# Performance work log

Hardware: AMD Instinct MI355X
Metric: run time of the kernel (lower is better)

## Reference

```python
import jax, jax.numpy as jnp
import numpy as np

N_NODES = 50000
DEG = 32
WIDTH = 128
DEPTH = 2
BATCH = 4096
EPS = 1e-12  # F.normalize default eps


def setup_inputs() -> dict:
    key = jax.random.key(0)
    k1, k2, k3, k4, k5, k6, k7 = jax.random.split(key, 7)
    nbd = jax.random.randint(k1, (N_NODES, DEG), 0, N_NODES, dtype=jnp.int32)
    node_idx = jax.random.randint(k2, (BATCH,), 0, N_NODES, dtype=jnp.int32)
    feats = jax.random.normal(k3, (BATCH, WIDTH), dtype=jnp.float32)
    s = 1.0 / np.sqrt(WIDTH)
    W_agg = jax.random.normal(k4, (WIDTH, WIDTH), dtype=jnp.float32) * s
    b_agg = jax.random.normal(k5, (WIDTH,), dtype=jnp.float32) * s
    W_lin = jax.random.normal(k6, (WIDTH, 2 * WIDTH), dtype=jnp.float32) * s
    b_lin = jax.random.normal(k7, (WIDTH,), dtype=jnp.float32) * s
    return {"nbd": nbd, "node_idx": node_idx, "feats": feats,
            "W_agg": W_agg, "b_agg": b_agg, "W_lin": W_lin, "b_lin": b_lin}


def reference(nbd, node_idx, feats, W_agg, b_agg, W_lin, b_lin):
    # H0: zero features for every graph node except the batch nodes (dict-of-zeros + row assignment in original)
    H = jnp.zeros((N_NODES, WIDTH), dtype=feats.dtype).at[node_idx].set(feats)
    for _ in range(DEPTH):  # combine Linear is weight-shared across hops (ModuleList([layer]*depth))
        # aggregator MLP applied once per node, then gathered per neighbor
        M = jax.nn.relu(H @ W_agg.T + b_agg)            # [N, d]
        agg = jnp.max(M[nbd], axis=1)                    # [N, deg, d] -> [N, d] max-pool aggregate
        h = jax.nn.relu(jnp.concatenate([H, agg], axis=-1) @ W_lin.T + b_lin)  # [N, d]
        norm = jnp.sqrt(jnp.sum(h * h, axis=-1, keepdims=True))
        H = h / jnp.maximum(norm, EPS)                   # F.normalize(dim=0) on 1d vector == per-row l2 norm
    return H[node_idx]                                   # [batch, width]
```

## Files before the change

kernel.cpp:

```cpp
#include <hip/hip_runtime.h>
#include <math.h>

#define N_NODES 50000
#define DEG 32
#define WIDTH 128
#define BATCH 4096
#define EPS 1e-12f

typedef __attribute__((ext_vector_type(8))) short short8;
typedef __attribute__((ext_vector_type(4))) float f32x4;
typedef unsigned short u16;

__device__ __forceinline__ u16 f2bf(float f) {
    unsigned x;
    __builtin_memcpy(&x, &f, 4);
    unsigned r = (x + 0x7fff + ((x >> 16) & 1)) >> 16;
    return (u16)r;
}
__device__ __forceinline__ unsigned pkmax_u16(unsigned a, unsigned b) {
    unsigned lo = (a & 0xffffu) > (b & 0xffffu) ? (a & 0xffffu) : (b & 0xffffu);
    unsigned hi = (a >> 16) > (b >> 16) ? (a >> 16) : (b >> 16);
    return lo | (hi << 16);
}

__global__ void prep_k(const float* __restrict__ W_agg, const float* __restrict__ W_lin,
                       const float* __restrict__ b_agg, int* __restrict__ inv,
                       u16* __restrict__ Wab, u16* __restrict__ Wlb,
                       unsigned* __restrict__ rbap) {
    int i = blockIdx.x * 256 + threadIdx.x;
    if (i < 50048) inv[i] = -1;
    int j = i - 50048;
    if (j >= 0 && j < 16384) Wab[j] = f2bf(W_agg[j]);
    int k = i - (50048 + 16384);
    if (k >= 0 && k < 32768) Wlb[k] = f2bf(W_lin[k]);
    if (i < 64) {
        float a = b_agg[2 * i], b = b_agg[2 * i + 1];
        a = a > 0.f ? a : 0.f;
        b = b > 0.f ? b : 0.f;
        rbap[i] = (unsigned)f2bf(a) | ((unsigned)f2bf(b) << 16);
    }
}

__global__ __launch_bounds__(512) void head_k(
    const float* __restrict__ feats, const u16* __restrict__ Wab, const u16* __restrict__ Wlb,
    const float* __restrict__ b_agg, const int* __restrict__ node_idx, int* __restrict__ inv,
    u16* __restrict__ M0b, float* __restrict__ S) {
    int tid = threadIdx.x;
    int gid = blockIdx.x * 512 + tid;
    if (gid < BATCH) atomicMax(&inv[node_idx[gid]], gid);

    int w = tid >> 6, l = tid & 63, li = l & 15, kq = l >> 4;
    int r0 = blockIdx.x * 16;
    int arow = r0 + li;
    int col = w * 16 + li;

    f32x4 am = (f32x4){0,0,0,0}, as = (f32x4){0,0,0,0};
#pragma unroll
    for (int kk = 0; kk < 4; ++kk) {
        float4 a0 = *(const float4*)(feats + (size_t)arow * 128 + kk * 32 + kq * 8);
        float4 a1 = *(const float4*)(feats + (size_t)arow * 128 + kk * 32 + kq * 8 + 4);
        short8 a;
        a[0] = (short)f2bf(a0.x); a[1] = (short)f2bf(a0.y);
        a[2] = (short)f2bf(a0.z); a[3] = (short)f2bf(a0.w);
        a[4] = (short)f2bf(a1.x); a[5] = (short)f2bf(a1.y);
        a[6] = (short)f2bf(a1.z); a[7] = (short)f2bf(a1.w);
        short8 bm = *(const short8*)(Wab + (size_t)col * 128 + kk * 32 + kq * 8);
        am = __builtin_amdgcn_mfma_f32_16x16x32_bf16(a, bm, am, 0, 0, 0);
        short8 bs = *(const short8*)(Wlb + (size_t)col * 256 + kk * 32 + kq * 8);
        as = __builtin_amdgcn_mfma_f32_16x16x32_bf16(a, bs, as, 0, 0, 0);
    }

    float ba = b_agg[col];
#pragma unroll
    for (int r = 0; r < 4; ++r) {
        int grow = r0 + kq * 4 + r;
        float t = am[r] + ba;
        t = t > 0.f ? t : 0.f;
        M0b[(size_t)grow * 128 + col] = f2bf(t);
        S[(size_t)grow * 128 + col] = as[r];
    }
}

__global__ __launch_bounds__(256) void agg1_k(
    const int* __restrict__ nbd, const int* __restrict__ inv,
    const u16* __restrict__ M0b, const unsigned* __restrict__ rbap,
    unsigned* __restrict__ AGG1u) {
    int wave = blockIdx.x * 4 + (threadIdx.x >> 6);
    int lane = threadIdx.x & 63;
    int n0 = wave * 2;

    int nb = nbd[(size_t)n0 * DEG + lane];
    int bi = inv[nb];
    unsigned long long warm = __ballot(bi >= 0);
    unsigned m0 = (unsigned)warm;
    unsigned m1 = (unsigned)(warm >> 32);

    unsigned rb = rbap[lane];

    unsigned acc0 = (m0 != 0xffffffffu) ? rb : 0u;
    while (m0) {
        int pos = __builtin_ctz(m0);
        m0 &= m0 - 1;
        int bib = __shfl(bi, pos);
        unsigned v = ((const unsigned*)(M0b + (size_t)bib * WIDTH))[lane];
        acc0 = pkmax_u16(acc0, v);
    }
    AGG1u[(size_t)n0 * 64 + lane] = acc0;

    unsigned acc1 = (m1 != 0xffffffffu) ? rb : 0u;
    while (m1) {
        int pos = __builtin_ctz(m1);
        m1 &= m1 - 1;
        int bib = __shfl(bi, 32 + pos);
        unsigned v = ((const unsigned*)(M0b + (size_t)bib * WIDTH))[lane];
        acc1 = pkmax_u16(acc1, v);
    }
    AGG1u[(size_t)(n0 + 1) * 64 + lane] = acc1;
}

__global__ __launch_bounds__(512) void hop1mm_k(
    const u16* __restrict__ AGG1, const int* __restrict__ inv,
    const float* __restrict__ S, const float* __restrict__ b_lin,
    const float* __restrict__ b_agg,
    const u16* __restrict__ Wlb, const u16* __restrict__ Wab,
    u16* __restrict__ H1g, u16* __restrict__ M1) {
    __shared__ u16 wlds[128 * 128];
    __shared__ u16 h1t[128 * 136];

    int tid = threadIdx.x;
    int w = tid >> 6, l = tid & 63, li = l & 15, kq = l >> 4;
    int row0 = blockIdx.x * 128;
    int lrow = w * 16 + li;
    int arow = row0 + lrow;
    if (arow > N_NODES - 1) arow = N_NODES - 1;

    short8 af[4];
#pragma unroll
    for (int kk = 0; kk < 4; ++kk)
        af[kk] = *(const short8*)(AGG1 + (size_t)arow * 128 + kk * 32 + kq * 8);

#pragma unroll
    for (int it = 0; it < 4; ++it) {
        int c = tid + it * 512;
        int r = c >> 4;
        int cb = (c & 15) << 4;
        short8 v = *(const short8*)(Wlb + (size_t)r * 256 + 128 + ((c & 15) << 3));
        *(short8*)((char*)wlds + r * 256 + (cb ^ ((r & 7) << 4))) = v;
    }
    __syncthreads();

    f32x4 h[8];
#pragma unroll
    for (int n = 0; n < 8; ++n) h[n] = (f32x4){0,0,0,0};
#pragma unroll
    for (int kk = 0; kk < 4; ++kk)
#pragma unroll
        for (int n = 0; n < 8; ++n) {
            int col = n * 16 + li;
            short8 b = *(const short8*)((char*)wlds + col * 256 +
                                        ((kk * 64 + kq * 16) ^ ((col & 7) << 4)));
            h[n] = __builtin_amdgcn_mfma_f32_16x16x32_bf16(af[kk], b, h[n], 0, 0, 0);
        }

    float blv[8];
#pragma unroll
    for (int n = 0; n < 8; ++n) blv[n] = b_lin[n * 16 + li];

#pragma unroll
    for (int r = 0; r < 4; ++r) {
        int lr = w * 16 + kq * 4 + r;
        int grow = row0 + lr;
        int growc = grow < N_NODES ? grow : N_NODES - 1;
        int bi = inv[growc];
        float v[8];
#pragma unroll
        for (int n = 0; n < 8; ++n) v[n] = h[n][r] + blv[n];
        if (bi >= 0) {
#pragma unroll
            for (int n = 0; n < 8; ++n) v[n] += S[(size_t)bi * 128 + n * 16 + li];
        }
        float p = 0.f;
#pragma unroll
        for (int n = 0; n < 8; ++n) {
            v[n] = fmaxf(v[n], 0.f);
            p += v[n] * v[n];
        }
        p += __shfl_xor(p, 1);
        p += __shfl_xor(p, 2);
        p += __shfl_xor(p, 4);
        p += __shfl_xor(p, 8);
        float sc = 1.0f / fmaxf(sqrtf(p), EPS);
        u16 vb[8];
#pragma unroll
        for (int n = 0; n < 8; ++n) vb[n] = f2bf(v[n] * sc);
        if (grow < N_NODES && bi >= 0) {
#pragma unroll
            for (int n = 0; n < 8; ++n) H1g[(size_t)grow * 128 + n * 16 + li] = vb[n];
        }
#pragma unroll
        for (int n = 0; n < 8; ++n) h1t[lr * 136 + n * 16 + li] = vb[n];
    }
    __syncthreads();

#pragma unroll
    for (int it = 0; it < 4; ++it) {
        int c = tid + it * 512;
        int r = c >> 4;
        int cb = (c & 15) << 4;
        short8 v = *(const short8*)(Wab + (size_t)r * 128 + ((c & 15) << 3));
        *(short8*)((char*)wlds + r * 256 + (cb ^ ((r & 7) << 4))) = v;
    }
    __syncthreads();

    short8 af2[4];
#pragma unroll
    for (int kk = 0; kk < 4; ++kk)
        af2[kk] = *(const short8*)(h1t + lrow * 136 + kk * 32 + kq * 8);

    f32x4 m[8];
#pragma unroll
    for (int n = 0; n < 8; ++n) m[n] = (f32x4){0,0,0,0};
#pragma unroll
    for (int kk = 0; kk < 4; ++kk)
#pragma unroll
        for (int n = 0; n < 8; ++n) {
            int col = n * 16 + li;
            short8 b = *(const short8*)((char*)wlds + col * 256 +
                                        ((kk * 64 + kq * 16) ^ ((col & 7) << 4)));
            m[n] = __builtin_amdgcn_mfma_f32_16x16x32_bf16(af2[kk], b, m[n], 0, 0, 0);
        }

    float bav[8];
#pragma unroll
    for (int n = 0; n < 8; ++n) bav[n] = b_agg[n * 16 + li];
#pragma unroll
    for (int r = 0; r < 4; ++r) {
        int grow = row0 + w * 16 + kq * 4 + r;
        if (grow < N_NODES) {
#pragma unroll
            for (int n = 0; n < 8; ++n) {
                float t = m[n][r] + bav[n];
                t = t > 0.f ? t : 0.f;
                M1[(size_t)grow * 128 + n * 16 + li] = f2bf(t);
            }
        }
    }
}

__global__ __launch_bounds__(512) void tail_k(
    const int* __restrict__ nbd, const int* __restrict__ node_idx,
    const u16* __restrict__ H1g, const u16* __restrict__ M1,
    const u16* __restrict__ Wlb, const float* __restrict__ b_lin,
    float* __restrict__ out) {
    __shared__ u16 ab2[16 * 264];
    __shared__ float pn[128];
    __shared__ float pnt[16];

    int tid = threadIdx.x;
    int w = tid >> 6, l = tid & 63, li = l & 15, kq = l >> 4;
    int row0 = blockIdx.x * 16;

#pragma unroll
    for (int rr = 0; rr < 2; ++rr) {
        int lr = w * 2 + rr;
        int i = row0 + lr;
        int n = node_idx[i];
        unsigned hv = ((const unsigned*)(H1g + (size_t)n * 128))[l];
        *(unsigned*)((char*)ab2 + lr * 528 + l * 4) = hv;
        int nb = (l < DEG) ? nbd[(size_t)n * DEG + l] : 0;
        unsigned acc = 0;
#pragma unroll
        for (int j = 0; j < DEG; ++j) {
            int bib = __shfl(nb, j);
            unsigned v = ((const unsigned*)(M1 + (size_t)bib * 128))[l];
            acc = pkmax_u16(acc, v);
        }
        *(unsigned*)((char*)ab2 + lr * 528 + 256 + l * 4) = acc;
    }
    __syncthreads();

    int col = w * 16 + li;
    f32x4 acc4 = (f32x4){0,0,0,0};
#pragma unroll
    for (int kk = 0; kk < 8; ++kk) {
        short8 a = *(const short8*)((char*)ab2 + li * 528 + kk * 64 + kq * 16);
        short8 b = *(const short8*)(Wlb + (size_t)col * 256 + kk * 32 + kq * 8);
        acc4 = __builtin_amdgcn_mfma_f32_16x16x32_bf16(a, b, acc4, 0, 0, 0);
    }

    float bl = b_lin[col];
    float v[4];
#pragma unroll
    for (int r = 0; r < 4; ++r) {
        v[r] = fmaxf(acc4[r] + bl, 0.f);
        float p = v[r] * v[r];
        p += __shfl_xor(p, 1);
        p += __shfl_xor(p, 2);
        p += __shfl_xor(p, 4);
        p += __shfl_xor(p, 8);
        if (li == 0) pn[w * 16 + kq * 4 + r] = p;
    }
    __syncthreads();
    if (tid < 16) {
        float s = 0.f;
#pragma unroll
        for (int ww = 0; ww < 8; ++ww) s += pn[ww * 16 + tid];
        pnt[tid] = s;
    }
    __syncthreads();
#pragma unroll
    for (int r = 0; r < 4; ++r) {
        int row = kq * 4 + r;
        float sc = 1.0f / fmaxf(sqrtf(pnt[row]), EPS);
        out[(size_t)(row0 + row) * 128 + col] = v[r] * sc;
    }
}

extern "C" void kernel_launch(void* const* d_in, const int* in_sizes, int n_in,
                              void* d_out, int out_size, void* d_ws, size_t ws_size,
                              hipStream_t stream) {
    const int*   nbd      = (const int*)d_in[0];
    const int*   node_idx = (const int*)d_in[1];
    const float* feats    = (const float*)d_in[2];
    const float* W_agg    = (const float*)d_in[3];
    const float* b_agg    = (const float*)d_in[4];
    const float* W_lin    = (const float*)d_in[5];
    const float* b_lin    = (const float*)d_in[6];
    float* out = (float*)d_out;

    char* base = (char*)d_ws;
    size_t off = 0;
    int* inv       = (int*)(base + off);      off += 50048 * 4;
    u16* Wab       = (u16*)(base + off);      off += 16384 * 2;
    u16* Wlb       = (u16*)(base + off);      off += 32768 * 2;
    unsigned* rbap = (unsigned*)(base + off); off += 64 * 4;
    u16* M0b       = (u16*)(base + off);      off += (size_t)BATCH * 128 * 2;
    float* S       = (float*)(base + off);    off += (size_t)BATCH * 128 * 4;
    u16* AGG1      = (u16*)(base + off);      off += (size_t)N_NODES * 128 * 2;
    u16* H1g       = (u16*)(base + off);      off += (size_t)N_NODES * 128 * 2;
    u16* M1        = (u16*)(base + off);      off += (size_t)N_NODES * 128 * 2;

    prep_k<<<(50048 + 16384 + 32768 + 255) / 256, 256, 0, stream>>>(
        W_agg, W_lin, b_agg, inv, Wab, Wlb, rbap);

    head_k<<<BATCH / 16, 512, 0, stream>>>(feats, Wab, Wlb, b_agg, node_idx, inv, M0b, S);

    agg1_k<<<N_NODES / 8, 256, 0, stream>>>(nbd, inv, M0b, rbap, (unsigned*)AGG1);

    hop1mm_k<<<(N_NODES + 127) / 128, 512, 0, stream>>>(
        AGG1, inv, S, b_lin, b_agg, Wlb, Wab, H1g, M1);

    tail_k<<<BATCH / 16, 512, 0, stream>>>(nbd, node_idx, H1g, M1, Wlb, b_lin, out);
}
```

Baseline: 54.88 us.

## Fuse hop-1 neighbor max aggregation into hop1 matmul kernel via LDS

The separate agg1 kernel, which wrote a 50000x128 bf16 AGG1 buffer to global memory, is removed. Each hop1mm block now computes the max-pool aggregate for its 128 rows directly into shared memory, reusing the LDS buffer that later holds H1. This cuts one kernel launch and the global write and read of AGG1. In exchange each 512-thread block does serial gather loops before its MFMA work, which may lower latency hiding compared with the smaller, more numerous agg1 blocks.

```diff
diff --git a/kernel.cpp b/kernel.cpp
--- a/kernel.cpp
+++ b/kernel.cpp
@@ -81,63 +81,21 @@
     }
 }
 
-__global__ __launch_bounds__(256) void agg1_k(
+__global__ __launch_bounds__(512) void hop1mm_k(
     const int* __restrict__ nbd, const int* __restrict__ inv,
     const u16* __restrict__ M0b, const unsigned* __restrict__ rbap,
-    unsigned* __restrict__ AGG1u) {
-    int wave = blockIdx.x * 4 + (threadIdx.x >> 6);
-    int lane = threadIdx.x & 63;
-    int n0 = wave * 2;
-
-    int nb = nbd[(size_t)n0 * DEG + lane];
-    int bi = inv[nb];
-    unsigned long long warm = __ballot(bi >= 0);
-    unsigned m0 = (unsigned)warm;
-    unsigned m1 = (unsigned)(warm >> 32);
-
-    unsigned rb = rbap[lane];
-
-    unsigned acc0 = (m0 != 0xffffffffu) ? rb : 0u;
-    while (m0) {
-        int pos = __builtin_ctz(m0);
-        m0 &= m0 - 1;
-        int bib = __shfl(bi, pos);
-        unsigned v = ((const unsigned*)(M0b + (size_t)bib * WIDTH))[lane];
-        acc0 = pkmax_u16(acc0, v);
-    }
-    AGG1u[(size_t)n0 * 64 + lane] = acc0;
-
-    unsigned acc1 = (m1 != 0xffffffffu) ? rb : 0u;
-    while (m1) {
-        int pos = __builtin_ctz(m1);
-        m1 &= m1 - 1;
-        int bib = __shfl(bi, 32 + pos);
-        unsigned v = ((const unsigned*)(M0b + (size_t)bib * WIDTH))[lane];
-        acc1 = pkmax_u16(acc1, v);
-    }
-    AGG1u[(size_t)(n0 + 1) * 64 + lane] = acc1;
-}
-
-__global__ __launch_bounds__(512) void hop1mm_k(
-    const u16* __restrict__ AGG1, const int* __restrict__ inv,
     const float* __restrict__ S, const float* __restrict__ b_lin,
     const float* __restrict__ b_agg,
     const u16* __restrict__ Wlb, const u16* __restrict__ Wab,
     u16* __restrict__ H1g, u16* __restrict__ M1) {
     __shared__ u16 wlds[128 * 128];
-    __shared__ u16 h1t[128 * 136];
+    __shared__ u16 sbuf[128 * 136];
+    unsigned* aggt = (unsigned*)sbuf;
 
     int tid = threadIdx.x;
     int w = tid >> 6, l = tid & 63, li = l & 15, kq = l >> 4;
     int row0 = blockIdx.x * 128;
     int lrow = w * 16 + li;
-    int arow = row0 + lrow;
-    if (arow > N_NODES - 1) arow = N_NODES - 1;
-
-    short8 af[4];
-#pragma unroll
-    for (int kk = 0; kk < 4; ++kk)
-        af[kk] = *(const short8*)(AGG1 + (size_t)arow * 128 + kk * 32 + kq * 8);
 
 #pragma unroll
     for (int it = 0; it < 4; ++it) {
@@ -147,6 +105,43 @@
         short8 v = *(const short8*)(Wlb + (size_t)r * 256 + 128 + ((c & 15) << 3));
         *(short8*)((char*)wlds + r * 256 + (cb ^ ((r & 7) << 4))) = v;
     }
+
+    unsigned rb = rbap[l];
+#pragma unroll
+    for (int p = 0; p < 8; ++p) {
+        int lr = w * 16 + p * 2;
+        int n0 = row0 + lr;
+        if (n0 > N_NODES - 2) n0 = N_NODES - 2;
+        int nb = nbd[(size_t)n0 * DEG + l];
+        int bi = inv[nb];
+        unsigned long long warm = __ballot(bi >= 0);
+        unsigned m0 = (unsigned)warm;
+        unsigned m1 = (unsigned)(warm >> 32);
+
+        unsigned acc0 = (m0 != 0xffffffffu) ? rb : 0u;
+        while (m0) {
+            int pos = __builtin_ctz(m0);
+            m0 &= m0 - 1;
+            int bib = __shfl(bi, pos);
+            acc0 = pkmax_u16(acc0, ((const unsigned*)(M0b + (size_t)bib * WIDTH))[l]);
+        }
+        aggt[lr * 68 + l] = acc0;
+
+        unsigned acc1 = (m1 != 0xffffffffu) ? rb : 0u;
+        while (m1) {
+            int pos = __builtin_ctz(m1);
+            m1 &= m1 - 1;
+            int bib = __shfl(bi, 32 + pos);
+            acc1 = pkmax_u16(acc1, ((const unsigned*)(M0b + (size_t)bib * WIDTH))[l]);
+        }
+        aggt[(lr + 1) * 68 + l] = acc1;
+    }
+    __syncthreads();
+
+    short8 af[4];
+#pragma unroll
+    for (int kk = 0; kk < 4; ++kk)
+        af[kk] = *(const short8*)(sbuf + lrow * 136 + kk * 32 + kq * 8);
     __syncthreads();
 
     f32x4 h[8];
@@ -198,7 +193,7 @@
             for (int n = 0; n < 8; ++n) H1g[(size_t)grow * 128 + n * 16 + li] = vb[n];
         }
 #pragma unroll
-        for (int n = 0; n < 8; ++n) h1t[lr * 136 + n * 16 + li] = vb[n];
+        for (int n = 0; n < 8; ++n) sbuf[lr * 136 + n * 16 + li] = vb[n];
     }
     __syncthreads();
 
@@ -215,7 +210,7 @@
     short8 af2[4];
 #pragma unroll
     for (int kk = 0; kk < 4; ++kk)
-        af2[kk] = *(const short8*)(h1t + lrow * 136 + kk * 32 + kq * 8);
+        af2[kk] = *(const short8*)(sbuf + lrow * 136 + kk * 32 + kq * 8);
 
     f32x4 m[8];
 #pragma unroll
@@ -272,8 +267,7 @@
 #pragma unroll
         for (int j = 0; j < DEG; ++j) {
             int bib = __shfl(nb, j);
-            unsigned v = ((const unsigned*)(M1 + (size_t)bib * 128))[l];
-            acc = pkmax_u16(acc, v);
+            acc = pkmax_u16(acc, ((const unsigned*)(M1 + (size_t)bib * 128))[l]);
         }
         *(unsigned*)((char*)ab2 + lr * 528 + 256 + l * 4) = acc;
     }
@@ -336,7 +330,6 @@
     unsigned* rbap = (unsigned*)(base + off); off += 64 * 4;
     u16* M0b       = (u16*)(base + off);      off += (size_t)BATCH * 128 * 2;
     float* S       = (float*)(base + off);    off += (size_t)BATCH * 128 * 4;
-    u16* AGG1      = (u16*)(base + off);      off += (size_t)N_NODES * 128 * 2;
     u16* H1g       = (u16*)(base + off);      off += (size_t)N_NODES * 128 * 2;
     u16* M1        = (u16*)(base + off);      off += (size_t)N_NODES * 128 * 2;
 
@@ -345,10 +338,8 @@
 
     head_k<<<BATCH / 16, 512, 0, stream>>>(feats, Wab, Wlb, b_agg, node_idx, inv, M0b, S);
 
-    agg1_k<<<N_NODES / 8, 256, 0, stream>>>(nbd, inv, M0b, rbap, (unsigned*)AGG1);
-
     hop1mm_k<<<(N_NODES + 127) / 128, 512, 0, stream>>>(
-        AGG1, inv, S, b_lin, b_agg, Wlb, Wab, H1g, M1);
+        nbd, inv, M0b, rbap, S, b_lin, b_agg, Wlb, Wab, H1g, M1);
 
     tail_k<<<BATCH / 16, 512, 0, stream>>>(nbd, node_idx, H1g, M1, Wlb, b_lin, out);
 }
```

Result: slower. 60.86 us (+10.9%).

## Remove weight-prep kernel; convert fp32 weights to bf16 inside each consumer kernel

Applied to the files above, without the earlier changes.

Drops the separate prep kernel that converted W_agg/W_lin to bf16 and initialised the inverse index. Each consumer kernel now loads the fp32 weights and converts them into swizzled LDS tiles itself, and the inverse map is set with hipMemsetAsync. The aim is to save one kernel launch and its serialisation. The cost is redundant fp32 weight reads and conversion in every block; head_k and tail_k now use large LDS buffers (64KB+), which may reduce occupancy.

```diff
diff --git a/kernel.cpp b/kernel.cpp
--- a/kernel.cpp
+++ b/kernel.cpp
@@ -22,52 +22,57 @@
     unsigned hi = (a >> 16) > (b >> 16) ? (a >> 16) : (b >> 16);
     return lo | (hi << 16);
 }
-
-__global__ void prep_k(const float* __restrict__ W_agg, const float* __restrict__ W_lin,
-                       const float* __restrict__ b_agg, int* __restrict__ inv,
-                       u16* __restrict__ Wab, u16* __restrict__ Wlb,
-                       unsigned* __restrict__ rbap) {
-    int i = blockIdx.x * 256 + threadIdx.x;
-    if (i < 50048) inv[i] = -1;
-    int j = i - 50048;
-    if (j >= 0 && j < 16384) Wab[j] = f2bf(W_agg[j]);
-    int k = i - (50048 + 16384);
-    if (k >= 0 && k < 32768) Wlb[k] = f2bf(W_lin[k]);
-    if (i < 64) {
-        float a = b_agg[2 * i], b = b_agg[2 * i + 1];
-        a = a > 0.f ? a : 0.f;
-        b = b > 0.f ? b : 0.f;
-        rbap[i] = (unsigned)f2bf(a) | ((unsigned)f2bf(b) << 16);
-    }
+__device__ __forceinline__ short8 cvt8(const float* __restrict__ p) {
+    float4 a0 = *(const float4*)p;
+    float4 a1 = *(const float4*)(p + 4);
+    short8 v;
+    v[0] = (short)f2bf(a0.x); v[1] = (short)f2bf(a0.y);
+    v[2] = (short)f2bf(a0.z); v[3] = (short)f2bf(a0.w);
+    v[4] = (short)f2bf(a1.x); v[5] = (short)f2bf(a1.y);
+    v[6] = (short)f2bf(a1.z); v[7] = (short)f2bf(a1.w);
+    return v;
 }
 
 __global__ __launch_bounds__(512) void head_k(
-    const float* __restrict__ feats, const u16* __restrict__ Wab, const u16* __restrict__ Wlb,
-    const float* __restrict__ b_agg, const int* __restrict__ node_idx, int* __restrict__ inv,
+    const float* __restrict__ feats, const float* __restrict__ W_agg,
+    const float* __restrict__ W_lin, const float* __restrict__ b_agg,
+    const int* __restrict__ node_idx, int* __restrict__ inv,
     u16* __restrict__ M0b, float* __restrict__ S) {
+    __shared__ u16 wa[128 * 128];
+    __shared__ u16 wl[128 * 128];
+
     int tid = threadIdx.x;
     int gid = blockIdx.x * 512 + tid;
     if (gid < BATCH) atomicMax(&inv[node_idx[gid]], gid);
+
+#pragma unroll
+    for (int it = 0; it < 4; ++it) {
+        int c = tid + it * 512;
+        int r = c >> 4, ch = c & 15;
+        int sw = (ch * 16) ^ ((r & 7) << 4);
+        *(short8*)((char*)wa + r * 256 + sw) = cvt8(W_agg + (size_t)r * 128 + ch * 8);
+        *(short8*)((char*)wl + r * 256 + sw) = cvt8(W_lin + (size_t)r * 256 + ch * 8);
+    }
 
     int w = tid >> 6, l = tid & 63, li = l & 15, kq = l >> 4;
     int r0 = blockIdx.x * 16;
     int arow = r0 + li;
     int col = w * 16 + li;
 
+    short8 a[4];
+#pragma unroll
+    for (int kk = 0; kk < 4; ++kk)
+        a[kk] = cvt8(feats + (size_t)arow * 128 + kk * 32 + kq * 8);
+    __syncthreads();
+
     f32x4 am = (f32x4){0,0,0,0}, as = (f32x4){0,0,0,0};
 #pragma unroll
     for (int kk = 0; kk < 4; ++kk) {
-        float4 a0 = *(const float4*)(feats + (size_t)arow * 128 + kk * 32 + kq * 8);
-        float4 a1 = *(const float4*)(feats + (size_t)arow * 128 + kk * 32 + kq * 8 + 4);
-        short8 a;
-        a[0] = (short)f2bf(a0.x); a[1] = (short)f2bf(a0.y);
-        a[2] = (short)f2bf(a0.z); a[3] = (short)f2bf(a0.w);
-        a[4] = (short)f2bf(a1.x); a[5] = (short)f2bf(a1.y);
-        a[6] = (short)f2bf(a1.z); a[7] = (short)f2bf(a1.w);
-        short8 bm = *(const short8*)(Wab + (size_t)col * 128 + kk * 32 + kq * 8);
-        am = __builtin_amdgcn_mfma_f32_16x16x32_bf16(a, bm, am, 0, 0, 0);
-        short8 bs = *(const short8*)(Wlb + (size_t)col * 256 + kk * 32 + kq * 8);
-        as = __builtin_amdgcn_mfma_f32_16x16x32_bf16(a, bs, as, 0, 0, 0);
+        int sw = (kk * 64 + kq * 16) ^ ((col & 7) << 4);
+        short8 bm = *(const short8*)((char*)wa + col * 256 + sw);
+        am = __builtin_amdgcn_mfma_f32_16x16x32_bf16(a[kk], bm, am, 0, 0, 0);
+        short8 bs = *(const short8*)((char*)wl + col * 256 + sw);
+        as = __builtin_amdgcn_mfma_f32_16x16x32_bf16(a[kk], bs, as, 0, 0, 0);
     }
 
     float ba = b_agg[col];
@@ -83,7 +88,7 @@
 
 __global__ __launch_bounds__(256) void agg1_k(
     const int* __restrict__ nbd, const int* __restrict__ inv,
-    const u16* __restrict__ M0b, const unsigned* __restrict__ rbap,
+    const u16* __restrict__ M0b, const float* __restrict__ b_agg,
     unsigned* __restrict__ AGG1u) {
     int wave = blockIdx.x * 4 + (threadIdx.x >> 6);
     int lane = threadIdx.x & 63;
@@ -95,15 +100,17 @@
     unsigned m0 = (unsigned)warm;
     unsigned m1 = (unsigned)(warm >> 32);
 
-    unsigned rb = rbap[lane];
+    float ba0 = b_agg[2 * lane], ba1 = b_agg[2 * lane + 1];
+    ba0 = ba0 > 0.f ? ba0 : 0.f;
+    ba1 = ba1 > 0.f ? ba1 : 0.f;
+    unsigned rb = (unsigned)f2bf(ba0) | ((unsigned)f2bf(ba1) << 16);
 
     unsigned acc0 = (m0 != 0xffffffffu) ? rb : 0u;
     while (m0) {
         int pos = __builtin_ctz(m0);
         m0 &= m0 - 1;
         int bib = __shfl(bi, pos);
-        unsigned v = ((const unsigned*)(M0b + (size_t)bib * WIDTH))[lane];
-        acc0 = pkmax_u16(acc0, v);
+        acc0 = pkmax_u16(acc0, ((const unsigned*)(M0b + (size_t)bib * WIDTH))[lane]);
     }
     AGG1u[(size_t)n0 * 64 + lane] = acc0;
 
@@ -112,8 +119,7 @@
         int pos = __builtin_ctz(m1);
         m1 &= m1 - 1;
         int bib = __shfl(bi, 32 + pos);
-        unsigned v = ((const unsigned*)(M0b + (size_t)bib * WIDTH))[lane];
-        acc1 = pkmax_u16(acc1, v);
+        acc1 = pkmax_u16(acc1, ((const unsigned*)(M0b + (size_t)bib * WIDTH))[lane]);
     }
     AGG1u[(size_t)(n0 + 1) * 64 + lane] = acc1;
 }
@@ -122,7 +128,7 @@
     const u16* __restrict__ AGG1, const int* __restrict__ inv,
     const float* __restrict__ S, const float* __restrict__ b_lin,
     const float* __restrict__ b_agg,
-    const u16* __restrict__ Wlb, const u16* __restrict__ Wab,
+    const float* __restrict__ W_lin, const float* __restrict__ W_agg,
     u16* __restrict__ H1g, u16* __restrict__ M1) {
     __shared__ u16 wlds[128 * 128];
     __shared__ u16 h1t[128 * 136];
@@ -142,10 +148,9 @@
 #pragma unroll
     for (int it = 0; it < 4; ++it) {
         int c = tid + it * 512;
-        int r = c >> 4;
-        int cb = (c & 15) << 4;
-        short8 v = *(const short8*)(Wlb + (size_t)r * 256 + 128 + ((c & 15) << 3));
-        *(short8*)((char*)wlds + r * 256 + (cb ^ ((r & 7) << 4))) = v;
+        int r = c >> 4, ch = c & 15;
+        *(short8*)((char*)wlds + r * 256 + ((ch * 16) ^ ((r & 7) << 4))) =
+            cvt8(W_lin + (size_t)r * 256 + 128 + ch * 8);
     }
     __syncthreads();
 
@@ -205,10 +210,9 @@
 #pragma unroll
     for (int it = 0; it < 4; ++it) {
         int c = tid + it * 512;
-        int r = c >> 4;
-        int cb = (c & 15) << 4;
-        short8 v = *(const short8*)(Wab + (size_t)r * 128 + ((c & 15) << 3));
-        *(short8*)((char*)wlds + r * 256 + (cb ^ ((r & 7) << 4))) = v;
+        int r = c >> 4, ch = c & 15;
+        *(short8*)((char*)wlds + r * 256 + ((ch * 16) ^ ((r & 7) << 4))) =
+            cvt8(W_agg + (size_t)r * 128 + ch * 8);
     }
     __syncthreads();
 
@@ -250,8 +254,9 @@
 __global__ __launch_bounds__(512) void tail_k(
     const int* __restrict__ nbd, const int* __restrict__ node_idx,
     const u16* __restrict__ H1g, const u16* __restrict__ M1,
-    const u16* __restrict__ Wlb, const float* __restrict__ b_lin,
+    const float* __restrict__ W_lin, const float* __restrict__ b_lin,
     float* __restrict__ out) {
+    __shared__ u16 wt[128 * 256];
     __shared__ u16 ab2[16 * 264];
     __shared__ float pn[128];
     __shared__ float pnt[16];
@@ -259,6 +264,14 @@
     int tid = threadIdx.x;
     int w = tid >> 6, l = tid & 63, li = l & 15, kq = l >> 4;
     int row0 = blockIdx.x * 16;
+
+#pragma unroll
+    for (int it = 0; it < 8; ++it) {
+        int c = tid + it * 512;
+        int r = c >> 5, ch = c & 31;
+        *(short8*)((char*)wt + r * 512 + ((ch * 16) ^ ((r & 7) << 4))) =
+            cvt8(W_lin + (size_t)r * 256 + ch * 8);
+    }
 
 #pragma unroll
     for (int rr = 0; rr < 2; ++rr) {
@@ -272,8 +285,7 @@
 #pragma unroll
         for (int j = 0; j < DEG; ++j) {
             int bib = __shfl(nb, j);
-            unsigned v = ((const unsigned*)(M1 + (size_t)bib * 128))[l];
-            acc = pkmax_u16(acc, v);
+            acc = pkmax_u16(acc, ((const unsigned*)(M1 + (size_t)bib * 128))[l]);
         }
         *(unsigned*)((char*)ab2 + lr * 528 + 256 + l * 4) = acc;
     }
@@ -284,7 +296,8 @@
 #pragma unroll
     for (int kk = 0; kk < 8; ++kk) {
         short8 a = *(const short8*)((char*)ab2 + li * 528 + kk * 64 + kq * 16);
-        short8 b = *(const short8*)(Wlb + (size_t)col * 256 + kk * 32 + kq * 8);
+        short8 b = *(const short8*)((char*)wt + col * 512 +
+                                    ((kk * 64 + kq * 16) ^ ((col & 7) << 4)));
         acc4 = __builtin_amdgcn_mfma_f32_16x16x32_bf16(a, b, acc4, 0, 0, 0);
     }
 
@@ -330,25 +343,21 @@
 
     char* base = (char*)d_ws;
     size_t off = 0;
-    int* inv       = (int*)(base + off);      off += 50048 * 4;
-    u16* Wab       = (u16*)(base + off);      off += 16384 * 2;
-    u16* Wlb       = (u16*)(base + off);      off += 32768 * 2;
-    unsigned* rbap = (unsigned*)(base + off); off += 64 * 4;
-    u16* M0b       = (u16*)(base + off);      off += (size_t)BATCH * 128 * 2;
-    float* S       = (float*)(base + off);    off += (size_t)BATCH * 128 * 4;
-    u16* AGG1      = (u16*)(base + off);      off += (size_t)N_NODES * 128 * 2;
-    u16* H1g       = (u16*)(base + off);      off += (size_t)N_NODES * 128 * 2;
-    u16* M1        = (u16*)(base + off);      off += (size_t)N_NODES * 128 * 2;
-
-    prep_k<<<(50048 + 16384 + 32768 + 255) / 256, 256, 0, stream>>>(
-        W_agg, W_lin, b_agg, inv, Wab, Wlb, rbap);
-
-    head_k<<<BATCH / 16, 512, 0, stream>>>(feats, Wab, Wlb, b_agg, node_idx, inv, M0b, S);
-
-    agg1_k<<<N_NODES / 8, 256, 0, stream>>>(nbd, inv, M0b, rbap, (unsigned*)AGG1);
+    int* inv  = (int*)(base + off);  off += 50048 * 4;
+    u16* M0b  = (u16*)(base + off);  off += (size_t)BATCH * 128 * 2;
+    float* S  = (float*)(base + off); off += (size_t)BATCH * 128 * 4;
+    u16* AGG1 = (u16*)(base + off);  off += (size_t)N_NODES * 128 * 2;
+    u16* H1g  = (u16*)(base + off);  off += (size_t)N_NODES * 128 * 2;
+    u16* M1   = (u16*)(base + off);  off += (size_t)N_NODES * 128 * 2;
+
+    hipMemsetAsync(inv, 0xFF, 50048 * 4, stream);
+
+    head_k<<<BATCH / 16, 512, 0, stream>>>(feats, W_agg, W_lin, b_agg, node_idx, inv, M0b, S);
+
+    agg1_k<<<N_NODES / 8, 256, 0, stream>>>(nbd, inv, M0b, b_agg, (unsigned*)AGG1);
 
     hop1mm_k<<<(N_NODES + 127) / 128, 512, 0, stream>>>(
-        AGG1, inv, S, b_lin, b_agg, Wlb, Wab, H1g, M1);
-
-    tail_k<<<BATCH / 16, 512, 0, stream>>>(nbd, node_idx, H1g, M1, Wlb, b_lin, out);
-}
+        AGG1, inv, S, b_lin, b_agg, W_lin, W_agg, H1g, M1);
+
+    tail_k<<<BATCH / 16, 512, 0, stream>>>(nbd, node_idx, H1g, M1, W_lin, b_lin, out);
+}
```

Measured after the change: 55.38 us. No clear change (+0.9%).
